# Performance work log

Measured on AMD Instinct MI355X. Metric: run time of the kernel, lower is better.

Reference implementation:

```python
import jax, jax.numpy as jnp
import numpy as np

HQ, HKV, D = 16, 2, 128   # num_heads_q, num_heads_kv, head_dim
G = HQ // HKV             # q heads per kv head (repeat_interleave factor)


def setup_inputs() -> dict:
    key = jax.random.key(0)
    ks = jax.random.split(key, 6)
    B, T, C = 2, 2048, 2048
    def w(k, shape):
        return jax.random.normal(k, shape, jnp.float32) * (1.0 / np.sqrt(shape[0]).astype(np.float32))
    x = jax.random.normal(ks[0], (B, T, C), jnp.float32)
    Wq = w(ks[1], (C, HQ * D))
    Wk = w(ks[2], (C, HKV * D))
    Wv = w(ks[3], (C, HKV * D))
    Wo = w(ks[4], (HQ * D, C))
    Wg = w(ks[5], (C, HQ))
    # causal mask: True where attention is disallowed (j > i)
    mask = jnp.triu(jnp.ones((T, T), dtype=bool), k=1)[None, None]  # (1,1,T,T)
    return {"x": x, "mask": mask, "Wq": Wq, "Wk": Wk, "Wv": Wv, "Wo": Wo, "Wg": Wg}


def reference(x, mask, Wq, Wk, Wv, Wo, Wg):
    B, T, C = x.shape
    # repeat_interleave(G, dim=heads) means q head h uses kv head h // G,
    # so group q heads as (HKV, G) instead of materializing repeated K/V.
    q = (x @ Wq).reshape(B, T, HKV, G, D).transpose(0, 2, 3, 1, 4)  # (B,HKV,G,T,D)
    k = (x @ Wk).reshape(B, T, HKV, D).transpose(0, 2, 1, 3)        # (B,HKV,T,D)
    v = (x @ Wv).reshape(B, T, HKV, D).transpose(0, 2, 1, 3)        # (B,HKV,T,D)
    scale = jnp.float32(1.0 / np.sqrt(D))
    scores = jnp.einsum('bkgtd,bksd->bkgts', q, k) * scale          # (B,HKV,G,T,T)
    scores = jnp.where(mask[:, None], jnp.float32(-1e9), scores)    # causal fill
    attn = jax.nn.softmax(scores, axis=-1)
    # post-softmax sigmoid gate, one scalar per (batch, q-head, query token)
    gates = jax.nn.sigmoid(x @ Wg)                                   # (B,T,HQ)
    gates = gates.transpose(0, 2, 1).reshape(B, HKV, G, T)           # (B,HKV,G,T)
    out = jnp.einsum('bkgts,bksd->btkgd', attn * gates[..., None], v)
    out = out.reshape(B, T, HQ * D)
    return out @ Wo
```

## Files before the change

kernel.cpp:

```cpp
#include <hip/hip_runtime.h>
#include <hip/hip_bf16.h>
#include <math.h>

#define HQ 16
#define HKV 2
#define D 128
#define B_SZ 2
#define T_SZ 2048
#define C_SZ 2048
#define QKVN 2688

typedef __attribute__((ext_vector_type(8))) short short8;
typedef __attribute__((ext_vector_type(4))) float floatx4;

static __device__ __forceinline__ float fexp2(float x) {
    return __builtin_amdgcn_exp2f(x);
}

static __device__ __forceinline__ unsigned short f2b(float f) {
    union { float f; unsigned u; } x; x.f = f;
    return (unsigned short)((x.u + 0x7fffu + ((x.u >> 16) & 1u)) >> 16);
}

static __device__ __forceinline__ unsigned int pk2(float a, float b) {
    float2 t; t.x = a; t.y = b;
    __hip_bfloat162 h = __float22bfloat162_rn(t);
    return *(unsigned int*)&h;
}

static __device__ __forceinline__ void load_lds16(const void* g, void* l) {
    __builtin_amdgcn_global_load_lds(
        (const __attribute__((address_space(1))) void*)g,
        (__attribute__((address_space(3))) void*)l,
        16, 0, 0);
}

__global__ __launch_bounds__(256) void f32_to_bf16_k(
    const float* __restrict__ in, unsigned short* __restrict__ out)
{
    int i = (blockIdx.x * 256 + threadIdx.x) * 8;
    float4 a = *(const float4*)(in + i);
    float4 b = *(const float4*)(in + i + 4);
    ushort4 o0, o1;
    o0.x = f2b(a.x); o0.y = f2b(a.y); o0.z = f2b(a.z); o0.w = f2b(a.w);
    o1.x = f2b(b.x); o1.y = f2b(b.y); o1.z = f2b(b.z); o1.w = f2b(b.w);
    *(ushort4*)(out + i) = o0;
    *(ushort4*)(out + i + 4) = o1;
}

__global__ __launch_bounds__(256) void transpose_f32_bf16(
    const float* __restrict__ in, unsigned short* __restrict__ out,
    int R, int Cc, float premul)
{
    __shared__ float t[32][33];
    const int bc = blockIdx.x * 32, br = blockIdx.y * 32;
    const int tid = threadIdx.x;
    const int r = tid >> 3, c4 = (tid & 7) * 4;
    float4 v = *(const float4*)(in + (size_t)(br + r) * Cc + bc + c4);
    t[r][c4 + 0] = v.x; t[r][c4 + 1] = v.y; t[r][c4 + 2] = v.z; t[r][c4 + 3] = v.w;
    __syncthreads();
    ushort4 o;
    o.x = f2b(t[c4 + 0][r] * premul); o.y = f2b(t[c4 + 1][r] * premul);
    o.z = f2b(t[c4 + 2][r] * premul); o.w = f2b(t[c4 + 3][r] * premul);
    *(ushort4*)(out + (size_t)(bc + r) * R + br + c4) = o;
}

__global__ __launch_bounds__(256) void wg_transpose(
    const float* __restrict__ Wg, unsigned short* __restrict__ out, float premul)
{
    int k = blockIdx.x * 256 + threadIdx.x;
    const float4* wr = (const float4*)(Wg + (size_t)k * 16);
    float4 w0 = wr[0], w1 = wr[1], w2 = wr[2], w3 = wr[3];
    float w[16] = {w0.x, w0.y, w0.z, w0.w, w1.x, w1.y, w1.z, w1.w,
                   w2.x, w2.y, w2.z, w2.w, w3.x, w3.y, w3.z, w3.w};
    #pragma unroll
    for (int h = 0; h < 16; ++h)
        out[(size_t)h * C_SZ + k] = f2b(w[h] * premul);
}

__global__ __launch_bounds__(256) void transpose_bf16_str(
    const unsigned short* __restrict__ in, unsigned short* __restrict__ out,
    int R, int Cc, int istr, long long ibstr, long long obstr)
{
    __shared__ unsigned short t[32][36];
    const int bz = blockIdx.z;
    const int bc = blockIdx.x * 32, br = blockIdx.y * 32;
    const int tid = threadIdx.x;
    const int r = tid >> 3, c4 = (tid & 7) * 4;
    ushort4 v = *(const ushort4*)(in + (size_t)bz * ibstr + (size_t)(br + r) * istr + bc + c4);
    t[r][c4 + 0] = v.x; t[r][c4 + 1] = v.y; t[r][c4 + 2] = v.z; t[r][c4 + 3] = v.w;
    __syncthreads();
    ushort4 o;
    o.x = t[c4 + 0][r]; o.y = t[c4 + 1][r]; o.z = t[c4 + 2][r]; o.w = t[c4 + 3][r];
    *(ushort4*)(out + (size_t)bz * obstr + (size_t)(bc + r) * R + br + c4) = o;
}

__global__ __launch_bounds__(256) void gemm_bt_bf16(
    const unsigned short* __restrict__ A, const unsigned short* __restrict__ Bt,
    float* __restrict__ Cf, unsigned short* __restrict__ Cb,
    int M, int N, int K, int out_bf16)
{
    __shared__ unsigned short As[128 * 32];
    __shared__ unsigned short Bs[128 * 32];
    const int tid = threadIdx.x;
    const int lane = tid & 63, wave = tid >> 6;
    const int l15 = lane & 15, quad = lane >> 4;
    const int wr = wave >> 1, wc = wave & 1;
    const int bm = blockIdx.y * 128, bn = blockIdx.x * 128;

    floatx4 zero = {0.f, 0.f, 0.f, 0.f};
    floatx4 acc[4][4];
    #pragma unroll
    for (int i = 0; i < 4; ++i)
        #pragma unroll
        for (int j = 0; j < 4; ++j) acc[i][j] = zero;

    int arow[2], acol[2];
    #pragma unroll
    for (int it = 0; it < 2; ++it) {
        int idx = it * 256 + tid;
        int row = idx >> 2, sb = idx & 3;
        int cb = sb ^ ((row >> 1) & 3);
        arow[it] = row; acol[it] = cb * 8;
    }
    const int sw = quad ^ ((l15 >> 1) & 3);

    for (int k0 = 0; k0 < K; k0 += 32) {
        __syncthreads();
        #pragma unroll
        for (int it = 0; it < 2; ++it) {
            load_lds16(A  + (size_t)(bm + arow[it]) * K + k0 + acol[it],
                       &As[(it * 256 + wave * 64) * 8]);
            load_lds16(Bt + (size_t)(bn + arow[it]) * K + k0 + acol[it],
                       &Bs[(it * 256 + wave * 64) * 8]);
        }
        __syncthreads();

        short8 af[4], bf[4];
        #pragma unroll
        for (int mt = 0; mt < 4; ++mt)
            af[mt] = *(const short8*)&As[((wr * 64 + mt * 16 + l15) * 4 + sw) * 8];
        #pragma unroll
        for (int nt = 0; nt < 4; ++nt)
            bf[nt] = *(const short8*)&Bs[((wc * 64 + nt * 16 + l15) * 4 + sw) * 8];
        #pragma unroll
        for (int mt = 0; mt < 4; ++mt)
            #pragma unroll
            for (int nt = 0; nt < 4; ++nt)
                acc[mt][nt] = __builtin_amdgcn_mfma_f32_16x16x32_bf16(
                    af[mt], bf[nt], acc[mt][nt], 0, 0, 0);
    }

    #pragma unroll
    for (int mt = 0; mt < 4; ++mt)
        #pragma unroll
        for (int nt = 0; nt < 4; ++nt)
            #pragma unroll
            for (int r = 0; r < 4; ++r) {
                int m = bm + wr * 64 + mt * 16 + quad * 4 + r;
                int n = bn + wc * 64 + nt * 16 + l15;
                if (out_bf16) Cb[(size_t)m * N + n] = f2b(acc[mt][nt][r]);
                else          Cf[(size_t)m * N + n] = acc[mt][nt][r];
            }
}

__global__ __launch_bounds__(256) void attn_mfma(
    const unsigned short* __restrict__ QKV, const unsigned short* __restrict__ Vt,
    unsigned short* __restrict__ Ob)
{
    __shared__ __align__(16) unsigned short SMEM[64 * 128 + 128 * 64 + 4 * 16 * 72];
    unsigned short* Ks = SMEM;
    unsigned short* Vs = SMEM + 64 * 128;
    unsigned short* Ps = SMEM + 64 * 128 + 128 * 64;
    unsigned short* Lo = SMEM;

    const int bh = blockIdx.x;
    const int qt = (int)gridDim.y - 1 - (int)blockIdx.y;
    const int b = bh >> 4, h = bh & 15, kvh = h >> 3;
    const int tid = threadIdx.x;
    const int lane = tid & 63, w = tid >> 6;
    const int l15 = lane & 15, quad = lane >> 4;
    const int q_local = w * 16 + l15;
    const float BIAS = 32.0f;

    short8 aq[4];
    {
        const unsigned short* qp = QKV + (size_t)(b * T_SZ + qt * 64 + q_local) * QKVN
                                       + h * D + quad * 8;
        #pragma unroll
        for (int kd = 0; kd < 4; ++kd) aq[kd] = *(const short8*)(qp + kd * 32);
    }

    const unsigned short* kg[4];
    const unsigned short* vg[4];
    #pragma unroll
    for (int it = 0; it < 4; ++it) {
        int Bi = it * 256 + tid;
        int kr = Bi >> 4, kc = ((Bi & 15) ^ (kr & 15)) * 8;
        kg[it] = QKV + (size_t)(b * T_SZ + kr) * QKVN + HQ * D + kvh * D + kc;
        int vr = Bi >> 3, vc = ((Bi & 7) ^ (vr & 7)) * 8;
        vg[it] = Vt + (size_t)((b * HKV + kvh) * D + vr) * T_SZ + vc;
    }

    floatx4 zero = {0.f, 0.f, 0.f, 0.f};
    floatx4 oacc[8];
    #pragma unroll
    for (int dt = 0; dt < 8; ++dt) oacc[dt] = zero;
    float l_part = 0.f;

    for (int kt = 0; kt <= qt; ++kt) {
        __syncthreads();
        #pragma unroll
        for (int it = 0; it < 4; ++it) {
            load_lds16(kg[it] + (size_t)kt * 64 * QKVN, &Ks[(it * 256 + w * 64) * 8]);
            load_lds16(vg[it] + kt * 64,                &Vs[(it * 256 + w * 64) * 8]);
        }
        __syncthreads();

        floatx4 sacc[4];
        #pragma unroll
        for (int nt = 0; nt < 4; ++nt) sacc[nt] = zero;
        #pragma unroll
        for (int kd = 0; kd < 4; ++kd)
            #pragma unroll
            for (int nt = 0; nt < 4; ++nt) {
                short8 ak = *(const short8*)&Ks[((nt * 16 + l15) * 16 + ((kd * 4 + quad) ^ l15)) * 8];
                sacc[nt] = __builtin_amdgcn_mfma_f32_16x16x32_bf16(ak, aq[kd], sacc[nt], 0, 0, 0);
            }

        float p[4][4];
        if (kt == qt) {
            #pragma unroll
            for (int nt = 0; nt < 4; ++nt)
                #pragma unroll
                for (int r = 0; r < 4; ++r) {
                    float e = fexp2(sacc[nt][r] - BIAS);
                    p[nt][r] = (nt * 16 + quad * 4 + r > q_local) ? 0.f : e;
                }
        } else {
            #pragma unroll
            for (int nt = 0; nt < 4; ++nt)
                #pragma unroll
                for (int r = 0; r < 4; ++r)
                    p[nt][r] = fexp2(sacc[nt][r] - BIAS);
        }
        #pragma unroll
        for (int nt = 0; nt < 4; ++nt) {
            l_part += (p[nt][0] + p[nt][1]) + (p[nt][2] + p[nt][3]);
            uint2 pw;
            pw.x = pk2(p[nt][0], p[nt][1]);
            pw.y = pk2(p[nt][2], p[nt][3]);
            *(uint2*)&Ps[(w * 16 + l15) * 72 + nt * 16 + quad * 4] = pw;
        }

        #pragma unroll
        for (int kk = 0; kk < 2; ++kk) {
            short8 bp = *(const short8*)&Ps[(w * 16 + l15) * 72 + kk * 32 + quad * 8];
            #pragma unroll
            for (int dt = 0; dt < 8; ++dt) {
                short8 av = *(const short8*)&Vs[((dt * 16 + l15) * 8 + ((kk * 4 + quad) ^ (l15 & 7))) * 8];
                oacc[dt] = __builtin_amdgcn_mfma_f32_16x16x32_bf16(av, bp, oacc[dt], 0, 0, 0);
            }
        }
    }

    float l = l_part;
    l += __shfl_xor(l, 16);
    l += __shfl_xor(l, 32);

    __syncthreads();
    {
        int token = b * T_SZ + qt * 64 + q_local;
        unsigned short gl = QKV[(size_t)token * QKVN + HQ * D + HKV * D * 2 + h];
        union { unsigned u; float f; } gx; gx.u = ((unsigned)gl) << 16;
        float g = 1.0f / (1.0f + fexp2(-gx.f));
        float f = g / l;
        #pragma unroll
        for (int dt = 0; dt < 8; ++dt) {
            uint2 ov;
            ov.x = pk2(oacc[dt][0] * f, oacc[dt][1] * f);
            ov.y = pk2(oacc[dt][2] * f, oacc[dt][3] * f);
            *(uint2*)&Lo[(size_t)q_local * 136 + dt * 16 + quad * 4] = ov;
        }
    }
    __syncthreads();
    {
        int row = tid >> 2, c0 = (tid & 3) * 32;
        size_t tok = (size_t)(b * T_SZ + qt * 64 + row);
        unsigned short* op = Ob + tok * (HQ * D) + h * D + c0;
        const unsigned short* lp = &Lo[(size_t)row * 136 + c0];
        short8 v0 = *(const short8*)(lp + 0);
        short8 v1 = *(const short8*)(lp + 8);
        short8 v2 = *(const short8*)(lp + 16);
        short8 v3 = *(const short8*)(lp + 24);
        *(short8*)(op + 0)  = v0; *(short8*)(op + 8)  = v1;
        *(short8*)(op + 16) = v2; *(short8*)(op + 24) = v3;
    }
}

extern "C" void kernel_launch(void* const* d_in, const int* in_sizes, int n_in,
                              void* d_out, int out_size, void* d_ws, size_t ws_size,
                              hipStream_t stream) {
    const float* x  = (const float*)d_in[0];
    const float* Wq = (const float*)d_in[2];
    const float* Wk = (const float*)d_in[3];
    const float* Wv = (const float*)d_in[4];
    const float* Wo = (const float*)d_in[5];
    const float* Wg = (const float*)d_in[6];
    float* out = (float*)d_out;

    const size_t KB = 1ull << 10;
    char* p = (char*)d_ws;
    unsigned short* xb    = (unsigned short*)(p);
    unsigned short* Ob    = xb;
    unsigned short* Wqkvt = (unsigned short*)(p + 16384 * KB);
    unsigned short* Wot   = (unsigned short*)(p + 27136 * KB);
    unsigned short* QKV   = (unsigned short*)(p + 35328 * KB);
    unsigned short* Vt    = (unsigned short*)(p + 56832 * KB);
    const int BT = B_SZ * T_SZ;

    const float c_q = (float)(0.08838834764831845 * 1.4426950408889634);
    const float c_g = 1.4426950408889634f;

    f32_to_bf16_k<<<dim3(BT * C_SZ / 2048), 256, 0, stream>>>(x, xb);
    transpose_f32_bf16<<<dim3(64, 64), 256, 0, stream>>>(Wq, Wqkvt, C_SZ, HQ * D, c_q);
    transpose_f32_bf16<<<dim3(8, 64), 256, 0, stream>>>(
        Wk, Wqkvt + (size_t)(HQ * D) * C_SZ, C_SZ, HKV * D, 1.0f);
    transpose_f32_bf16<<<dim3(8, 64), 256, 0, stream>>>(
        Wv, Wqkvt + (size_t)(HQ * D + HKV * D) * C_SZ, C_SZ, HKV * D, 1.0f);
    wg_transpose<<<dim3(8), 256, 0, stream>>>(
        Wg, Wqkvt + (size_t)(HQ * D + 2 * HKV * D) * C_SZ, c_g);
    transpose_f32_bf16<<<dim3(64, 64), 256, 0, stream>>>(Wo, Wot, HQ * D, C_SZ, 1.0f);

    gemm_bt_bf16<<<dim3(QKVN / 128, BT / 128), 256, 0, stream>>>(
        xb, Wqkvt, nullptr, QKV, BT, QKVN, C_SZ, 1);

    transpose_bf16_str<<<dim3((HKV * D) / 32, T_SZ / 32, B_SZ), 256, 0, stream>>>(
        QKV + HQ * D + HKV * D, Vt, T_SZ, HKV * D, QKVN,
        (long long)T_SZ * QKVN, (long long)(HKV * D) * T_SZ);

    attn_mfma<<<dim3(B_SZ * HQ, T_SZ / 64), 256, 0, stream>>>(QKV, Vt, Ob);

    gemm_bt_bf16<<<dim3(C_SZ / 128, BT / 128), 256, 0, stream>>>(
        Ob, Wot, out, nullptr, BT, C_SZ, HQ * D, 0);
}
```

Baseline: 327.9 us.

## Merge prep kernels into one launch and fuse V transpose into QKV GEMM epilogue

Six preprocessing launches (x cast plus the Wq, Wk, Wv, Wo and Wg transpose-casts) become one prep_kernel that picks its role from the block index. The standalone V transpose kernel is removed. The QKV GEMM blocks that cover the V columns now write V^T directly through LDS staging instead of writing V into QKV. This cuts launch overhead and an extra read and write of V, at the cost of a larger shared buffer and a branchy epilogue in those GEMM blocks.

```diff
diff --git a/kernel.cpp b/kernel.cpp
--- a/kernel.cpp
+++ b/kernel.cpp
@@ -10,6 +10,9 @@
 #define C_SZ 2048
 #define QKVN 2688
 
+#define C_Q 0.12753102f
+#define C_G 1.44269504f
+
 typedef __attribute__((ext_vector_type(8))) short short8;
 typedef __attribute__((ext_vector_type(4))) float floatx4;
 
@@ -35,25 +38,11 @@
         16, 0, 0);
 }
 
-__global__ __launch_bounds__(256) void f32_to_bf16_k(
-    const float* __restrict__ in, unsigned short* __restrict__ out)
+static __device__ __forceinline__ void tr32(
+    const float* __restrict__ in, unsigned short* __restrict__ out,
+    int R, int Cc, float premul, int bx, int by, float (*t)[33])
 {
-    int i = (blockIdx.x * 256 + threadIdx.x) * 8;
-    float4 a = *(const float4*)(in + i);
-    float4 b = *(const float4*)(in + i + 4);
-    ushort4 o0, o1;
-    o0.x = f2b(a.x); o0.y = f2b(a.y); o0.z = f2b(a.z); o0.w = f2b(a.w);
-    o1.x = f2b(b.x); o1.y = f2b(b.y); o1.z = f2b(b.z); o1.w = f2b(b.w);
-    *(ushort4*)(out + i) = o0;
-    *(ushort4*)(out + i + 4) = o1;
-}
-
-__global__ __launch_bounds__(256) void transpose_f32_bf16(
-    const float* __restrict__ in, unsigned short* __restrict__ out,
-    int R, int Cc, float premul)
-{
-    __shared__ float t[32][33];
-    const int bc = blockIdx.x * 32, br = blockIdx.y * 32;
+    const int bc = bx * 32, br = by * 32;
     const int tid = threadIdx.x;
     const int r = tid >> 3, c4 = (tid & 7) * 4;
     float4 v = *(const float4*)(in + (size_t)(br + r) * Cc + bc + c4);
@@ -65,43 +54,58 @@
     *(ushort4*)(out + (size_t)(bc + r) * R + br + c4) = o;
 }
 
-__global__ __launch_bounds__(256) void wg_transpose(
-    const float* __restrict__ Wg, unsigned short* __restrict__ out, float premul)
+__global__ __launch_bounds__(256) void prep_kernel(
+    const float* __restrict__ x,  const float* __restrict__ Wq,
+    const float* __restrict__ Wk, const float* __restrict__ Wv,
+    const float* __restrict__ Wo, const float* __restrict__ Wg,
+    unsigned short* __restrict__ xb, unsigned short* __restrict__ Wqkvt,
+    unsigned short* __restrict__ Wot)
 {
-    int k = blockIdx.x * 256 + threadIdx.x;
-    const float4* wr = (const float4*)(Wg + (size_t)k * 16);
-    float4 w0 = wr[0], w1 = wr[1], w2 = wr[2], w3 = wr[3];
-    float w[16] = {w0.x, w0.y, w0.z, w0.w, w1.x, w1.y, w1.z, w1.w,
-                   w2.x, w2.y, w2.z, w2.w, w3.x, w3.y, w3.z, w3.w};
-    #pragma unroll
-    for (int h = 0; h < 16; ++h)
-        out[(size_t)h * C_SZ + k] = f2b(w[h] * premul);
-}
-
-__global__ __launch_bounds__(256) void transpose_bf16_str(
-    const unsigned short* __restrict__ in, unsigned short* __restrict__ out,
-    int R, int Cc, int istr, long long ibstr, long long obstr)
-{
-    __shared__ unsigned short t[32][36];
-    const int bz = blockIdx.z;
-    const int bc = blockIdx.x * 32, br = blockIdx.y * 32;
+    __shared__ float t[32][33];
+    const int bid = blockIdx.x;
     const int tid = threadIdx.x;
-    const int r = tid >> 3, c4 = (tid & 7) * 4;
-    ushort4 v = *(const ushort4*)(in + (size_t)bz * ibstr + (size_t)(br + r) * istr + bc + c4);
-    t[r][c4 + 0] = v.x; t[r][c4 + 1] = v.y; t[r][c4 + 2] = v.z; t[r][c4 + 3] = v.w;
-    __syncthreads();
-    ushort4 o;
-    o.x = t[c4 + 0][r]; o.y = t[c4 + 1][r]; o.z = t[c4 + 2][r]; o.w = t[c4 + 3][r];
-    *(ushort4*)(out + (size_t)bz * obstr + (size_t)(bc + r) * R + br + c4) = o;
+    if (bid < 4096) {
+        int i = bid * 2048 + tid * 8;
+        float4 a = *(const float4*)(x + i);
+        float4 b = *(const float4*)(x + i + 4);
+        ushort4 o0, o1;
+        o0.x = f2b(a.x); o0.y = f2b(a.y); o0.z = f2b(a.z); o0.w = f2b(a.w);
+        o1.x = f2b(b.x); o1.y = f2b(b.y); o1.z = f2b(b.z); o1.w = f2b(b.w);
+        *(ushort4*)(xb + i) = o0;
+        *(ushort4*)(xb + i + 4) = o1;
+    } else if (bid < 8192) {
+        int n = bid - 4096;
+        tr32(Wq, Wqkvt, C_SZ, HQ * D, C_Q, n & 63, n >> 6, t);
+    } else if (bid < 8704) {
+        int n = bid - 8192;
+        tr32(Wk, Wqkvt + (size_t)(HQ * D) * C_SZ, C_SZ, HKV * D, 1.0f, n & 7, n >> 3, t);
+    } else if (bid < 9216) {
+        int n = bid - 8704;
+        tr32(Wv, Wqkvt + (size_t)(HQ * D + HKV * D) * C_SZ, C_SZ, HKV * D, 1.0f, n & 7, n >> 3, t);
+    } else if (bid < 13312) {
+        int n = bid - 9216;
+        tr32(Wo, Wot, HQ * D, C_SZ, 1.0f, n & 63, n >> 6, t);
+    } else {
+        int k = (bid - 13312) * 256 + tid;
+        const float4* wr = (const float4*)(Wg + (size_t)k * 16);
+        float4 w0 = wr[0], w1 = wr[1], w2 = wr[2], w3 = wr[3];
+        float w[16] = {w0.x, w0.y, w0.z, w0.w, w1.x, w1.y, w1.z, w1.w,
+                       w2.x, w2.y, w2.z, w2.w, w3.x, w3.y, w3.z, w3.w};
+        unsigned short* out = Wqkvt + (size_t)(HQ * D + 2 * HKV * D) * C_SZ;
+        #pragma unroll
+        for (int h = 0; h < 16; ++h)
+            out[(size_t)h * C_SZ + k] = f2b(w[h] * C_G);
+    }
 }
 
 __global__ __launch_bounds__(256) void gemm_bt_bf16(
     const unsigned short* __restrict__ A, const unsigned short* __restrict__ Bt,
     float* __restrict__ Cf, unsigned short* __restrict__ Cb,
-    int M, int N, int K, int out_bf16)
+    unsigned short* __restrict__ Vt, int M, int N, int K, int out_bf16)
 {
-    __shared__ unsigned short As[128 * 32];
-    __shared__ unsigned short Bs[128 * 32];
+    __shared__ __align__(16) unsigned short SM[8448];
+    unsigned short* As = SM;
+    unsigned short* Bs = SM + 4096;
     const int tid = threadIdx.x;
     const int lane = tid & 63, wave = tid >> 6;
     const int l15 = lane & 15, quad = lane >> 4;
@@ -149,6 +153,38 @@
             for (int nt = 0; nt < 4; ++nt)
                 acc[mt][nt] = __builtin_amdgcn_mfma_f32_16x16x32_bf16(
                     af[mt], bf[nt], acc[mt][nt], 0, 0, 0);
+    }
+
+    if (Vt && (bn == 2304 || bn == 2432)) {
+        unsigned short (*Ct)[132] = (unsigned short(*)[132])SM;
+        const int bb = bm >> 11;
+        const int tl = bm & 2047;
+        #pragma unroll
+        for (int vn = 0; vn < 2; ++vn) {
+            __syncthreads();
+            if (wc == vn) {
+                #pragma unroll
+                for (int mt = 0; mt < 4; ++mt)
+                    #pragma unroll
+                    for (int nt = 0; nt < 4; ++nt)
+                        #pragma unroll
+                        for (int r = 0; r < 4; ++r)
+                            Ct[nt * 16 + l15][wr * 64 + mt * 16 + quad * 4 + r] =
+                                f2b(acc[mt][nt][r]);
+            }
+            __syncthreads();
+            int row = tid >> 2, cs = (tid & 3) * 32;
+            int vrow = (bn - 2304) + vn * 64 + row;
+            unsigned short* dst = Vt + ((size_t)bb * (HKV * D) + vrow) * T_SZ + tl + cs;
+            const unsigned short* src = &Ct[row][cs];
+            short8 v0 = *(const short8*)(src + 0);
+            short8 v1 = *(const short8*)(src + 8);
+            short8 v2 = *(const short8*)(src + 16);
+            short8 v3 = *(const short8*)(src + 24);
+            *(short8*)(dst + 0)  = v0; *(short8*)(dst + 8)  = v1;
+            *(short8*)(dst + 16) = v2; *(short8*)(dst + 24) = v3;
+        }
+        return;
     }
 
     #pragma unroll
@@ -319,28 +355,13 @@
     unsigned short* Vt    = (unsigned short*)(p + 56832 * KB);
     const int BT = B_SZ * T_SZ;
 
-    const float c_q = (float)(0.08838834764831845 * 1.4426950408889634);
-    const float c_g = 1.4426950408889634f;
-
-    f32_to_bf16_k<<<dim3(BT * C_SZ / 2048), 256, 0, stream>>>(x, xb);
-    transpose_f32_bf16<<<dim3(64, 64), 256, 0, stream>>>(Wq, Wqkvt, C_SZ, HQ * D, c_q);
-    transpose_f32_bf16<<<dim3(8, 64), 256, 0, stream>>>(
-        Wk, Wqkvt + (size_t)(HQ * D) * C_SZ, C_SZ, HKV * D, 1.0f);
-    transpose_f32_bf16<<<dim3(8, 64), 256, 0, stream>>>(
-        Wv, Wqkvt + (size_t)(HQ * D + HKV * D) * C_SZ, C_SZ, HKV * D, 1.0f);
-    wg_transpose<<<dim3(8), 256, 0, stream>>>(
-        Wg, Wqkvt + (size_t)(HQ * D + 2 * HKV * D) * C_SZ, c_g);
-    transpose_f32_bf16<<<dim3(64, 64), 256, 0, stream>>>(Wo, Wot, HQ * D, C_SZ, 1.0f);
+    prep_kernel<<<dim3(13320), 256, 0, stream>>>(x, Wq, Wk, Wv, Wo, Wg, xb, Wqkvt, Wot);
 
     gemm_bt_bf16<<<dim3(QKVN / 128, BT / 128), 256, 0, stream>>>(
-        xb, Wqkvt, nullptr, QKV, BT, QKVN, C_SZ, 1);
-
-    transpose_bf16_str<<<dim3((HKV * D) / 32, T_SZ / 32, B_SZ), 256, 0, stream>>>(
-        QKV + HQ * D + HKV * D, Vt, T_SZ, HKV * D, QKVN,
-        (long long)T_SZ * QKVN, (long long)(HKV * D) * T_SZ);
+        xb, Wqkvt, nullptr, QKV, Vt, BT, QKVN, C_SZ, 1);
 
     attn_mfma<<<dim3(B_SZ * HQ, T_SZ / 64), 256, 0, stream>>>(QKV, Vt, Ob);
 
     gemm_bt_bf16<<<dim3(C_SZ / 128, BT / 128), 256, 0, stream>>>(
-        Ob, Wot, out, nullptr, BT, C_SZ, HQ * D, 0);
-}
+        Ob, Wot, out, nullptr, nullptr, BT, C_SZ, HQ * D, 0);
+}
```

Result: faster. 314.2 us (-4.2%).
